# Performance work log

Measured on AMD Instinct MI355X. Metric: run time of the kernel, lower is better.

The kernel has to match this reference:

```python
import jax, jax.numpy as jnp
import numpy as np

T, D, H, E = 8192, 1024, 2048, 8


def setup_inputs() -> dict:
    key = jax.random.key(0)
    k1, k2, k3 = jax.random.split(key, 3)
    x = jax.random.normal(k1, (T, D), dtype=jnp.float32)
    # counts must sum to T; use a uniform split (reference handles any valid split)
    num_tokens_per_expert = jnp.full((E,), T // E, dtype=jnp.int32)
    w_up = jax.random.normal(k2, (E, H, D), dtype=jnp.float32) * (1.0 / np.sqrt(D))
    w_down = jax.random.normal(k3, (E, D, H), dtype=jnp.float32) * (1.0 / np.sqrt(H))
    return {"x": x, "num_tokens_per_expert": num_tokens_per_expert, "w_up": w_up, "w_down": w_down}


def reference(x, num_tokens_per_expert, w_up, w_down):
    """Grouped MoE expert MLP: per-expert  x @ w_up[e].T -> relu^2 -> @ w_down[e].T.
    Tokens are sorted by expert; counts encode the segment boundaries.
    Matches the CUDA path: bf16 compute for both GEMMs and the activation,
    final cast back to x.dtype.
    """
    n_tok = x.shape[0]
    n_exp = w_up.shape[0]
    # segment id per token from cumulative offsets (same as grouped_mm offs)
    offsets = jnp.cumsum(num_tokens_per_expert)  # (E,)
    expert_id = jnp.searchsorted(offsets, jnp.arange(n_tok), side="right")  # (T,)

    xb = x.astype(jnp.bfloat16)
    wu = w_up.astype(jnp.bfloat16)   # (E, H, D)
    wd = w_down.astype(jnp.bfloat16)  # (E, D, H)

    out = jnp.zeros((n_tok, x.shape[1]), dtype=jnp.bfloat16)
    # small fixed loop over experts; token dim fully vectorized
    for e in range(n_exp):
        h = jnp.maximum(xb @ wu[e].T, 0)          # (T, H) relu
        h = (h * h).astype(jnp.bfloat16)           # square, re-cast as original
        y = h @ wd[e].T                            # (T, D)
        out = out + jnp.where((expert_id == e)[:, None], y, jnp.bfloat16(0))
    return out.astype(x.dtype)
```

## Files before the change

### kernel.cpp

```cpp
#include <hip/hip_runtime.h>
#include <stdint.h>

constexpr int T_TOK = 8192;
constexpr int D_DIM = 1024;
constexpr int H_DIM = 2048;
constexpr int E_NUM = 8;

typedef __bf16 bf16x8 __attribute__((ext_vector_type(8)));
typedef float  f32x4  __attribute__((ext_vector_type(4)));
typedef unsigned int u32x4 __attribute__((ext_vector_type(4)));

static __device__ __forceinline__ unsigned short f2bf(float f) {
  union { float f; unsigned u; } a; a.f = f;
  unsigned r = a.u + 0x7fffu + ((a.u >> 16) & 1u);
  return (unsigned short)(r >> 16);
}
static __device__ __forceinline__ float bf2f(unsigned short h) {
  union { unsigned u; float f; } a; a.u = ((unsigned)h) << 16;
  return a.f;
}

__global__ void cvt_f32_bf16(const float* __restrict__ src,
                             unsigned short* __restrict__ dst, int n4) {
  int i = blockIdx.x * blockDim.x + threadIdx.x;
  int stride = gridDim.x * blockDim.x;
  for (; i < n4; i += stride) {
    float4 v = reinterpret_cast<const float4*>(src)[i];
    ushort4 o;
    o.x = f2bf(v.x); o.y = f2bf(v.y); o.z = f2bf(v.z); o.w = f2bf(v.w);
    reinterpret_cast<ushort4*>(dst)[i] = o;
  }
}

#define FENCE() asm volatile("" ::: "memory")
#define BARRIER() do { FENCE(); __builtin_amdgcn_s_barrier(); FENCE(); } while (0)
#define WAIT_LGKM0() asm volatile("s_waitcnt lgkmcnt(0)" ::: "memory")
#define WAIT_VM(N) asm volatile("s_waitcnt vmcnt(%0)" :: "i"(N) : "memory")
#define SCHED_FENCE() __builtin_amdgcn_sched_barrier(0)

static __device__ __forceinline__ f32x4 gload4(const void* p) {
  f32x4 r;
  asm volatile("global_load_dwordx4 %0, %1, off" : "=v"(r) : "v"(p) : "memory");
  return r;
}

template <int K_DIM, int N_DIM, int BN, bool RELU2>
__global__ __launch_bounds__(512, 2)
void gg8(const unsigned short* __restrict__ A,
         const float* __restrict__ Bw,
         const int* __restrict__ counts,
         void* __restrict__ Cout) {
  constexpr int BM = 256, BK = 64;
  constexpr int NT = K_DIM / BK;
  constexpr int WNC = BN / 4;
  constexpr int NACC = WNC / 16;
  constexpr int NQN = NACC / 2;
  constexpr int BL = (BN == 256) ? 4 : 2;
  constexpr int TSH = (BN == 256) ? 2 : 3;
  constexpr int FPB = BL * 16;

  const int tid  = threadIdx.x;
  const int wid  = tid >> 6;
  const int lane = tid & 63;
  const int wr   = wid >> 2;
  const int wc   = wid & 3;

  int t = blockIdx.x;
  int e = -1, rowBase = 0, rowsValid = 0;
  {
    int tiles = 0, off = 0;
#pragma unroll
    for (int i = 0; i < E_NUM; ++i) {
      int n  = counts[i];
      int nt = (n + BM - 1) / BM;
      if (e < 0 && t < tiles + nt) {
        e = i;
        int lt = t - tiles;
        rowBase   = off + lt * BM;
        rowsValid = n - lt * BM;
        if (rowsValid > BM) rowsValid = BM;
      }
      tiles += nt; off += n;
    }
  }
  if (e < 0) return;
  const int colBase = blockIdx.y * BN;

  __shared__ __align__(1024) char lds[(BM + BN) * BK * 2 * 2];
  auto ldsA = [&](int b) -> char* { return lds + b * (BM * 128); };
  auto ldsB = [&](int b) -> char* { return lds + 2 * (BM * 128) + b * (BN * 128); };

  const char* gA = (const char*)A + (size_t)rowBase * (K_DIM * 2);
  const int  bRow0 = tid >> TSH;
  const int  bByte = (tid & ((1 << TSH) - 1)) * FPB;
  const char* gBbase = (const char*)Bw +
      ((size_t)e * N_DIM + colBase) * (size_t)(K_DIM * 4);

  const int lr8 = lane >> 3;
  const int gsw = (lane & 7) ^ lr8;

  auto stageA = [&](int buf, int alpha, int kt) {
#pragma unroll
    for (int j = 0; j < 2; ++j) {
      int bi   = j * 8 + wid;
      int row0 = (bi >> 3) * 128 + alpha * 64 + (bi & 7) * 8;
      int sr   = row0 + lr8;
      if (sr >= rowsValid) sr = rowsValid - 1;
      const char* src = gA + (size_t)sr * (K_DIM * 2) + (size_t)kt * 128 + gsw * 16;
      __builtin_amdgcn_global_load_lds(
          (const __attribute__((address_space(1))) void*)src,
          (__attribute__((address_space(3))) void*)(ldsA(buf) + row0 * 128),
          16, 0, 0);
    }
  };

  auto loadBhalf = [&](f32x4 (&q)[BL], int h, int kt) {
    const char* s = gBbase + (size_t)(h * (BN / 2) + bRow0) * (K_DIM * 4)
                  + (size_t)kt * 256 + bByte;
#pragma unroll
    for (int j = 0; j < BL; ++j) q[j] = gload4(s + j * 16);
  };
  auto writeBhalf = [&](int buf, const f32x4 (&q)[BL], int h) {
    const int row = h * (BN / 2) + bRow0;
    char* base = ldsB(buf) + row * 128;
    const int rs = row & 7;
#pragma unroll
    for (int c = 0; c < BL / 2; ++c) {
      u32x4 w;
#pragma unroll
      for (int k = 0; k < 2; ++k) {
        const f32x4& v = q[c * 2 + k];
#pragma unroll
        for (int p = 0; p < 2; ++p) {
          unsigned lo = f2bf(v[p * 2]), hi = f2bf(v[p * 2 + 1]);
          w[k * 2 + p] = lo | (hi << 16);
        }
      }
      int g = (BN == 256) ? (2 * (tid & 3) + c) : (tid & 7);
      *reinterpret_cast<u32x4*>(base + (g ^ rs) * 16) = w;
    }
  };

  const int rowLane = lane & 15;
  const int grpA    = lane >> 4;
  const int swzm    = lane & 7;

  bf16x8 aF[4][2];
  bf16x8 bF0[NQN][2], bF1[NQN][2];
  f32x4  accC[8][NACC];
#pragma unroll
  for (int m = 0; m < 8; ++m)
#pragma unroll
    for (int n = 0; n < NACC; ++n) accC[m][n] = (f32x4){0.f, 0.f, 0.f, 0.f};

  auto readA = [&](int buf, int rh) {
    const char* base = ldsA(buf) + (wr * 128 + rh * 64 + rowLane) * 128;
#pragma unroll
    for (int m = 0; m < 4; ++m)
#pragma unroll
      for (int ks = 0; ks < 2; ++ks) {
        int g = (ks * 4 + grpA) ^ swzm;
        aF[m][ks] = *(const bf16x8*)(base + m * (16 * 128) + g * 16);
      }
  };
  auto readB = [&](int buf, int ch, bf16x8 (&dst)[NQN][2]) {
    const char* base = ldsB(buf) + (wc * WNC + ch * (WNC / 2) + rowLane) * 128;
#pragma unroll
    for (int n = 0; n < NQN; ++n)
#pragma unroll
      for (int ks = 0; ks < 2; ++ks) {
        int g = (ks * 4 + grpA) ^ swzm;
        dst[n][ks] = *(const bf16x8*)(base + n * (16 * 128) + g * 16);
      }
  };

#define MFMAQ(RH, CH, BFA)                                                    \
  do {                                                                        \
    __builtin_amdgcn_s_setprio(1);                                            \
    _Pragma("unroll")                                                         \
    for (int m_ = 0; m_ < 4; ++m_) {                                          \
      _Pragma("unroll")                                                       \
      for (int n_ = 0; n_ < NQN; ++n_) {                                      \
        f32x4 c_ = accC[(RH) * 4 + m_][(CH) * NQN + n_];                      \
        c_ = __builtin_amdgcn_mfma_f32_16x16x32_bf16(aF[m_][0], BFA[n_][0], c_, 0, 0, 0); \
        c_ = __builtin_amdgcn_mfma_f32_16x16x32_bf16(aF[m_][1], BFA[n_][1], c_, 0, 0, 0); \
        accC[(RH) * 4 + m_][(CH) * NQN + n_] = c_;                            \
      }                                                                       \
    }                                                                         \
    __builtin_amdgcn_s_setprio(0);                                            \
  } while (0)

  f32x4 bq0[BL], bq1[BL];

  loadBhalf(bq0, 0, 0);
  loadBhalf(bq1, 1, 0);
  stageA(0, 0, 0); stageA(0, 1, 0);
  WAIT_VM(BL + 4);  SCHED_FENCE();  writeBhalf(0, bq0, 0);
  WAIT_VM(4);       SCHED_FENCE();  writeBhalf(0, bq1, 1);
  WAIT_VM(0); WAIT_LGKM0();
  BARRIER();

  for (int t2 = 0; t2 < NT; ++t2) {
    const int cur = t2 & 1, nxt = cur ^ 1;
    const int ktn = (t2 + 1 < NT) ? t2 + 1 : NT - 1;

    loadBhalf(bq0, 0, ktn);
    readA(cur, 0); readB(cur, 0, bF0);
    BARRIER(); WAIT_LGKM0();
    MFMAQ(0, 0, bF0);
    BARRIER();

    loadBhalf(bq1, 1, ktn);
    stageA(nxt, 0, ktn);
    readB(cur, 1, bF1);
    BARRIER(); WAIT_LGKM0();
    MFMAQ(0, 1, bF1);
    WAIT_VM(2 * BL + 2);
    BARRIER();

    WAIT_VM(BL + 2);
    SCHED_FENCE();
    writeBhalf(nxt, bq0, 0);
    stageA(nxt, 1, ktn);
    readA(cur, 1);
    BARRIER(); WAIT_LGKM0();
    MFMAQ(1, 1, bF1);
    BARRIER();

    WAIT_VM(4);
    SCHED_FENCE();
    writeBhalf(nxt, bq1, 1);
    WAIT_VM(2);
    BARRIER(); WAIT_LGKM0();
    MFMAQ(1, 0, bF0);
    BARRIER();
  }

  const int rB0 = wr * 128 + grpA * 4;
  const int cB0 = colBase + wc * WNC + rowLane;
#pragma unroll
  for (int m = 0; m < 8; ++m) {
#pragma unroll
    for (int n = 0; n < NACC; ++n) {
#pragma unroll
      for (int j = 0; j < 4; ++j) {
        int r = rB0 + m * 16 + j;
        if (r < rowsValid) {
          size_t idx = (size_t)(rowBase + r) * N_DIM + (cB0 + n * 16);
          float v = accC[m][n][j];
          if (RELU2) {
            v = v > 0.f ? v : 0.f;
            float hb = bf2f(f2bf(v));
            ((unsigned short*)Cout)[idx] = f2bf(hb * hb);
          } else {
            ((float*)Cout)[idx] = bf2f(f2bf(v));
          }
        }
      }
    }
  }
#undef MFMAQ
}

extern "C" void kernel_launch(void* const* d_in, const int* in_sizes, int n_in,
                              void* d_out, int out_size, void* d_ws, size_t ws_size,
                              hipStream_t stream) {
  const float* x   = (const float*)d_in[0];
  const int*   cnt = (const int*)d_in[1];
  const float* wu  = (const float*)d_in[2];
  const float* wd  = (const float*)d_in[3];
  float* out = (float*)d_out;
  char*  ws  = (char*)d_ws;

  unsigned short* xb   = (unsigned short*)(ws);
  unsigned short* hbuf = (unsigned short*)(ws + (16u << 20));

  cvt_f32_bf16<<<2048, 256, 0, stream>>>(x, xb, T_TOK * D_DIM / 4);

  gg8<D_DIM, H_DIM, 256, true ><<<dim3(40, H_DIM / 256), dim3(512), 0, stream>>>(
      xb, wu, cnt, (void*)hbuf);
  gg8<H_DIM, D_DIM, 128, false><<<dim3(40, D_DIM / 128), dim3(512), 0, stream>>>(
      hbuf, wd, cnt, (void*)out);
}
```

Before: 126.9 us.

## Load fp32 weights straight into MFMA B registers, bypassing LDS

```diff
diff --git a/kernel.cpp b/kernel.cpp
--- a/kernel.cpp
+++ b/kernel.cpp
@@ -8,16 +8,11 @@
 
 typedef __bf16 bf16x8 __attribute__((ext_vector_type(8)));
 typedef float  f32x4  __attribute__((ext_vector_type(4)));
-typedef unsigned int u32x4 __attribute__((ext_vector_type(4)));
 
 static __device__ __forceinline__ unsigned short f2bf(float f) {
   union { float f; unsigned u; } a; a.f = f;
   unsigned r = a.u + 0x7fffu + ((a.u >> 16) & 1u);
   return (unsigned short)(r >> 16);
-}
-static __device__ __forceinline__ float bf2f(unsigned short h) {
-  union { unsigned u; float f; } a; a.u = ((unsigned)h) << 16;
-  return a.f;
 }
 
 __global__ void cvt_f32_bf16(const float* __restrict__ src,
@@ -34,7 +29,6 @@
 
 #define FENCE() asm volatile("" ::: "memory")
 #define BARRIER() do { FENCE(); __builtin_amdgcn_s_barrier(); FENCE(); } while (0)
-#define WAIT_LGKM0() asm volatile("s_waitcnt lgkmcnt(0)" ::: "memory")
 #define WAIT_VM(N) asm volatile("s_waitcnt vmcnt(%0)" :: "i"(N) : "memory")
 #define SCHED_FENCE() __builtin_amdgcn_sched_barrier(0)
 
@@ -44,20 +38,15 @@
   return r;
 }
 
-template <int K_DIM, int N_DIM, int BN, bool RELU2>
+template <int K_DIM, int N_DIM, bool RELU2>
 __global__ __launch_bounds__(512, 2)
-void gg8(const unsigned short* __restrict__ A,
+void gg9(const unsigned short* __restrict__ A,
          const float* __restrict__ Bw,
          const int* __restrict__ counts,
          void* __restrict__ Cout) {
-  constexpr int BM = 256, BK = 64;
+  constexpr int BM = 256, BN = 128, BK = 64;
   constexpr int NT = K_DIM / BK;
-  constexpr int WNC = BN / 4;
-  constexpr int NACC = WNC / 16;
-  constexpr int NQN = NACC / 2;
-  constexpr int BL = (BN == 256) ? 4 : 2;
-  constexpr int TSH = (BN == 256) ? 2 : 3;
-  constexpr int FPB = BL * 16;
+  constexpr int NACC = 2;
 
   const int tid  = threadIdx.x;
   const int wid  = tid >> 6;
@@ -86,15 +75,10 @@
   if (e < 0) return;
   const int colBase = blockIdx.y * BN;
 
-  __shared__ __align__(1024) char lds[(BM + BN) * BK * 2 * 2];
+  __shared__ __align__(1024) char lds[2 * BM * 128];
   auto ldsA = [&](int b) -> char* { return lds + b * (BM * 128); };
-  auto ldsB = [&](int b) -> char* { return lds + 2 * (BM * 128) + b * (BN * 128); };
 
   const char* gA = (const char*)A + (size_t)rowBase * (K_DIM * 2);
-  const int  bRow0 = tid >> TSH;
-  const int  bByte = (tid & ((1 << TSH) - 1)) * FPB;
-  const char* gBbase = (const char*)Bw +
-      ((size_t)e * N_DIM + colBase) * (size_t)(K_DIM * 4);
 
   const int lr8 = lane >> 3;
   const int gsw = (lane & 7) ^ lr8;
@@ -114,130 +98,113 @@
     }
   };
 
-  auto loadBhalf = [&](f32x4 (&q)[BL], int h, int kt) {
-    const char* s = gBbase + (size_t)(h * (BN / 2) + bRow0) * (K_DIM * 4)
-                  + (size_t)kt * 256 + bByte;
-#pragma unroll
-    for (int j = 0; j < BL; ++j) q[j] = gload4(s + j * 16);
-  };
-  auto writeBhalf = [&](int buf, const f32x4 (&q)[BL], int h) {
-    const int row = h * (BN / 2) + bRow0;
-    char* base = ldsB(buf) + row * 128;
-    const int rs = row & 7;
-#pragma unroll
-    for (int c = 0; c < BL / 2; ++c) {
-      u32x4 w;
-#pragma unroll
-      for (int k = 0; k < 2; ++k) {
-        const f32x4& v = q[c * 2 + k];
-#pragma unroll
-        for (int p = 0; p < 2; ++p) {
-          unsigned lo = f2bf(v[p * 2]), hi = f2bf(v[p * 2 + 1]);
-          w[k * 2 + p] = lo | (hi << 16);
-        }
-      }
-      int g = (BN == 256) ? (2 * (tid & 3) + c) : (tid & 7);
-      *reinterpret_cast<u32x4*>(base + (g ^ rs) * 16) = w;
-    }
-  };
-
   const int rowLane = lane & 15;
   const int grpA    = lane >> 4;
   const int swzm    = lane & 7;
 
-  bf16x8 aF[4][2];
-  bf16x8 bF0[NQN][2], bF1[NQN][2];
-  f32x4  accC[8][NACC];
+  const char* gBrow[NACC];
+#pragma unroll
+  for (int n = 0; n < NACC; ++n)
+    gBrow[n] = (const char*)Bw +
+        ((size_t)e * N_DIM + colBase + wc * 32 + n * 16 + rowLane) * (size_t)(K_DIM * 4)
+        + (size_t)grpA * 32;
+
+  auto loadB = [&](f32x4 (&q)[8], int kt) {
+#pragma unroll
+    for (int n = 0; n < NACC; ++n)
+#pragma unroll
+      for (int ks = 0; ks < 2; ++ks) {
+        const char* s = gBrow[n] + (size_t)kt * 256 + ks * 128;
+        q[n * 4 + ks * 2 + 0] = gload4(s);
+        q[n * 4 + ks * 2 + 1] = gload4(s + 16);
+      }
+  };
+  auto cvtB = [&](const f32x4 (&q)[8], int ks, bf16x8 (&bF)[NACC]) {
+#pragma unroll
+    for (int n = 0; n < NACC; ++n) {
+      union { __bf16 b[8]; bf16x8 v; } u;
+#pragma unroll
+      for (int j = 0; j < 2; ++j)
+#pragma unroll
+        for (int p = 0; p < 4; ++p)
+          u.b[j * 4 + p] = (__bf16)q[n * 4 + ks * 2 + j][p];
+      bF[n] = u.v;
+    }
+  };
+
+  f32x4 accC[8][NACC];
 #pragma unroll
   for (int m = 0; m < 8; ++m)
 #pragma unroll
     for (int n = 0; n < NACC; ++n) accC[m][n] = (f32x4){0.f, 0.f, 0.f, 0.f};
 
-  auto readA = [&](int buf, int rh) {
-    const char* base = ldsA(buf) + (wr * 128 + rh * 64 + rowLane) * 128;
-#pragma unroll
-    for (int m = 0; m < 4; ++m)
-#pragma unroll
-      for (int ks = 0; ks < 2; ++ks) {
-        int g = (ks * 4 + grpA) ^ swzm;
-        aF[m][ks] = *(const bf16x8*)(base + m * (16 * 128) + g * 16);
-      }
-  };
-  auto readB = [&](int buf, int ch, bf16x8 (&dst)[NQN][2]) {
-    const char* base = ldsB(buf) + (wc * WNC + ch * (WNC / 2) + rowLane) * 128;
-#pragma unroll
-    for (int n = 0; n < NQN; ++n)
-#pragma unroll
-      for (int ks = 0; ks < 2; ++ks) {
-        int g = (ks * 4 + grpA) ^ swzm;
-        dst[n][ks] = *(const bf16x8*)(base + n * (16 * 128) + g * 16);
-      }
-  };
-
-#define MFMAQ(RH, CH, BFA)                                                    \
+  auto readAks = [&](int buf, int ks, bf16x8 (&aF)[8]) {
+    const char* base = ldsA(buf) + (wr * 128 + rowLane) * 128;
+#pragma unroll
+    for (int m = 0; m < 8; ++m) {
+      int g = (ks * 4 + grpA) ^ swzm;
+      aF[m] = *(const bf16x8*)(base + m * (16 * 128) + g * 16);
+    }
+  };
+
+  f32x4 bqA[8], bqB[8];
+  bf16x8 aF[8], bF[NACC];
+
+  stageA(0, 0, 0); stageA(0, 1, 0);
+  SCHED_FENCE();
+  loadB(bqA, 0);
+  WAIT_VM(0);
+  SCHED_FENCE();
+  BARRIER();
+
+#define ITER(T, CUR, BQC, BQN)                                                \
   do {                                                                        \
+    const int ktn_ = ((T) + 1 < NT) ? (T) + 1 : NT - 1;                       \
+    stageA((CUR) ^ 1, 0, ktn_);                                               \
+    stageA((CUR) ^ 1, 1, ktn_);                                               \
+    SCHED_FENCE();                                                            \
+    loadB(BQN, ktn_);                                                         \
+    readAks(CUR, 0, aF);                                                      \
+    WAIT_VM(12);                                                              \
+    SCHED_FENCE();                                                            \
+    cvtB(BQC, 0, bF);                                                         \
     __builtin_amdgcn_s_setprio(1);                                            \
     _Pragma("unroll")                                                         \
-    for (int m_ = 0; m_ < 4; ++m_) {                                          \
+    for (int m_ = 0; m_ < 8; ++m_)                                            \
       _Pragma("unroll")                                                       \
-      for (int n_ = 0; n_ < NQN; ++n_) {                                      \
-        f32x4 c_ = accC[(RH) * 4 + m_][(CH) * NQN + n_];                      \
-        c_ = __builtin_amdgcn_mfma_f32_16x16x32_bf16(aF[m_][0], BFA[n_][0], c_, 0, 0, 0); \
-        c_ = __builtin_amdgcn_mfma_f32_16x16x32_bf16(aF[m_][1], BFA[n_][1], c_, 0, 0, 0); \
-        accC[(RH) * 4 + m_][(CH) * NQN + n_] = c_;                            \
-      }                                                                       \
-    }                                                                         \
+      for (int n_ = 0; n_ < NACC; ++n_)                                       \
+        accC[m_][n_] = __builtin_amdgcn_mfma_f32_16x16x32_bf16(               \
+            aF[m_], bF[n_], accC[m_][n_], 0, 0, 0);                           \
     __builtin_amdgcn_s_setprio(0);                                            \
+    readAks(CUR, 1, aF);                                                      \
+    cvtB(BQC, 1, bF);                                                         \
+    __builtin_amdgcn_s_setprio(1);                                            \
+    _Pragma("unroll")                                                         \
+    for (int m_ = 0; m_ < 8; ++m_)                                            \
+      _Pragma("unroll")                                                       \
+      for (int n_ = 0; n_ < NACC; ++n_)                                       \
+        accC[m_][n_] = __builtin_amdgcn_mfma_f32_16x16x32_bf16(               \
+            aF[m_], bF[n_], accC[m_][n_], 0, 0, 0);                           \
+    __builtin_amdgcn_s_setprio(0);                                            \
+    WAIT_VM(8);                                                               \
+    BARRIER();                                                                \
   } while (0)
 
-  f32x4 bq0[BL], bq1[BL];
-
-  loadBhalf(bq0, 0, 0);
-  loadBhalf(bq1, 1, 0);
-  stageA(0, 0, 0); stageA(0, 1, 0);
-  WAIT_VM(BL + 4);  SCHED_FENCE();  writeBhalf(0, bq0, 0);
-  WAIT_VM(4);       SCHED_FENCE();  writeBhalf(0, bq1, 1);
-  WAIT_VM(0); WAIT_LGKM0();
-  BARRIER();
-
-  for (int t2 = 0; t2 < NT; ++t2) {
-    const int cur = t2 & 1, nxt = cur ^ 1;
-    const int ktn = (t2 + 1 < NT) ? t2 + 1 : NT - 1;
-
-    loadBhalf(bq0, 0, ktn);
-    readA(cur, 0); readB(cur, 0, bF0);
-    BARRIER(); WAIT_LGKM0();
-    MFMAQ(0, 0, bF0);
-    BARRIER();
-
-    loadBhalf(bq1, 1, ktn);
-    stageA(nxt, 0, ktn);
-    readB(cur, 1, bF1);
-    BARRIER(); WAIT_LGKM0();
-    MFMAQ(0, 1, bF1);
-    WAIT_VM(2 * BL + 2);
-    BARRIER();
-
-    WAIT_VM(BL + 2);
-    SCHED_FENCE();
-    writeBhalf(nxt, bq0, 0);
-    stageA(nxt, 1, ktn);
-    readA(cur, 1);
-    BARRIER(); WAIT_LGKM0();
-    MFMAQ(1, 1, bF1);
-    BARRIER();
-
-    WAIT_VM(4);
-    SCHED_FENCE();
-    writeBhalf(nxt, bq1, 1);
-    WAIT_VM(2);
-    BARRIER(); WAIT_LGKM0();
-    MFMAQ(1, 0, bF0);
-    BARRIER();
+  for (int t2 = 0; t2 < NT; t2 += 2) {
+    ITER(t2,     0, bqA, bqB);
+    ITER(t2 + 1, 1, bqB, bqA);
+  }
+#undef ITER
+
+  WAIT_VM(0);
+  SCHED_FENCE();
+#pragma unroll
+  for (int j = 0; j < 8; ++j) {
+    asm volatile("" :: "v"(bqA[j]), "v"(bqB[j]));
   }
 
   const int rB0 = wr * 128 + grpA * 4;
-  const int cB0 = colBase + wc * WNC + rowLane;
+  const int cB0 = colBase + wc * 32 + rowLane;
 #pragma unroll
   for (int m = 0; m < 8; ++m) {
 #pragma unroll
@@ -249,17 +216,16 @@
           size_t idx = (size_t)(rowBase + r) * N_DIM + (cB0 + n * 16);
           float v = accC[m][n][j];
           if (RELU2) {
-            v = v > 0.f ? v : 0.f;
-            float hb = bf2f(f2bf(v));
-            ((unsigned short*)Cout)[idx] = f2bf(hb * hb);
+            float rl = v > 0.f ? v : 0.f;
+            float hf = (float)(__bf16)rl;
+            ((__bf16*)Cout)[idx] = (__bf16)(hf * hf);
           } else {
-            ((float*)Cout)[idx] = bf2f(f2bf(v));
+            ((float*)Cout)[idx] = (float)(__bf16)v;
           }
         }
       }
     }
   }
-#undef MFMAQ
 }
 
 extern "C" void kernel_launch(void* const* d_in, const int* in_sizes, int n_in,
@@ -277,8 +243,8 @@
 
   cvt_f32_bf16<<<2048, 256, 0, stream>>>(x, xb, T_TOK * D_DIM / 4);
 
-  gg8<D_DIM, H_DIM, 256, true ><<<dim3(40, H_DIM / 256), dim3(512), 0, stream>>>(
+  gg9<D_DIM, H_DIM, true ><<<dim3(40, H_DIM / 128), dim3(512), 0, stream>>>(
       xb, wu, cnt, (void*)hbuf);
-  gg8<H_DIM, D_DIM, 128, false><<<dim3(40, D_DIM / 128), dim3(512), 0, stream>>>(
+  gg9<H_DIM, D_DIM, false><<<dim3(40, D_DIM / 128), dim3(512), 0, stream>>>(
       hbuf, wd, cnt, (void*)out);
 }
```

Result: slower. 169.7 us (+33.8%).
